# Optimization experiments

Hardware: AMD Instinct MI355X
Metric: run time of the kernel (lower is better)

## Reference

```python
import jax, jax.numpy as jnp
import numpy as np

N_NODES = 100000
N_EDGES = 1600000  # directed, src < dst; to_undirected doubles them
N_GRAPHS = 128
D_IN, D_H, D_FC, N_CLS = 128, 64, 32, 10


def setup_inputs() -> dict:
    key = jax.random.key(0)
    ks = jax.random.split(key, 12)
    x = jax.random.normal(ks[0], (N_NODES, D_IN), dtype=jnp.float32)
    # edges with src < dst so concatenating the flipped copy yields the undirected set
    r = jax.random.randint(ks[1], (2, N_EDGES), 0, N_NODES, dtype=jnp.int64)
    src = jnp.minimum(r[0], r[1])
    dst = jnp.maximum(r[0], r[1])
    dst = jnp.where(src == dst, (dst + 1) % N_NODES, dst)  # avoid pre-existing self loops
    edge_index = jnp.stack([src, dst])
    batch = jnp.sort(jax.random.randint(ks[2], (N_NODES,), 0, N_GRAPHS, dtype=jnp.int64))
    sc = lambda f: 1.0 / jnp.sqrt(jnp.float32(f))
    return {
        "x": x,
        "edge_index": edge_index,
        "batch": batch,
        "W_in": jax.random.normal(ks[3], (D_IN, D_H), jnp.float32) * sc(D_IN),
        "b_in": jnp.zeros((D_H,), jnp.float32),
        "W1": jax.random.normal(ks[4], (D_H, D_H), jnp.float32) * sc(D_H),
        "b1": jnp.zeros((D_H,), jnp.float32),
        "W2": jax.random.normal(ks[5], (D_H, D_H), jnp.float32) * sc(D_H),
        "b2": jnp.zeros((D_H,), jnp.float32),
        "Wf1": jax.random.normal(ks[6], (D_H, D_FC), jnp.float32) * sc(D_H),
        "bf1": jnp.zeros((D_FC,), jnp.float32),
        "Wf2": jax.random.normal(ks[7], (D_FC, N_CLS), jnp.float32) * sc(D_FC),
        "bf2": jnp.zeros((N_CLS,), jnp.float32),
    }


def _gcn_conv(x, W, b, src, dst, dinv, n_nodes):
    # GCNConv: x' = D^{-1/2}(A+I)D^{-1/2} (xW) + b, dinv = deg^{-1/2} incl. self loops
    xw = x @ W
    norm = (dinv[src] * dinv[dst])[:, None]              # [E,1]
    agg = jax.ops.segment_sum(xw[src] * norm, dst, num_segments=n_nodes)
    agg = agg + xw * (dinv * dinv)[:, None]              # self-loop term
    return agg + b


def reference(x, edge_index, batch, W_in, b_in, W1, b1, W2, b2, Wf1, bf1, Wf2, bf2):
    n = x.shape[0]
    # to_undirected: append reversed edges (inputs have src<dst, so no dup dirs)
    src = jnp.concatenate([edge_index[0], edge_index[1]])
    dst = jnp.concatenate([edge_index[1], edge_index[0]])
    # degree including self loop
    deg = 1.0 + jax.ops.segment_sum(jnp.ones_like(dst, dtype=x.dtype), dst, num_segments=n)
    dinv = jax.lax.rsqrt(deg)

    h = jax.nn.relu(x @ W_in + b_in)
    h = jax.nn.relu(_gcn_conv(h, W1, b1, src, dst, dinv, n))
    h = jax.nn.relu(_gcn_conv(h, W2, b2, src, dst, dinv, n))

    # global_mean_pool over graph ids
    sums = jax.ops.segment_sum(h, batch, num_segments=N_GRAPHS)
    cnts = jax.ops.segment_sum(jnp.ones((n,), h.dtype), batch, num_segments=N_GRAPHS)
    pooled = sums / jnp.maximum(cnts, 1.0)[:, None]

    g = jax.nn.relu(pooled @ Wf1 + bf1)
    logits = g @ Wf2 + bf2
    return jax.nn.log_softmax(logits, axis=1)
```

## Files before the change

kernel.cpp:

```cpp
#include <hip/hip_runtime.h>
#include <hip/hip_fp16.h>
#include <math.h>

constexpr int DG  = 128;
constexpr int DIN = 128;
constexpr int DH  = 64;
constexpr int DFC = 32;
constexpr int DC  = 10;
constexpr int CAP  = 80;
constexpr int NPB  = 64;
constexpr int NB   = 1563;
constexpr int ABLK = 256;
constexpr int SCAP = 2560;

typedef _Float16 f16;
typedef f16  f16x8 __attribute__((ext_vector_type(8)));
typedef float f32x4 __attribute__((ext_vector_type(4)));

__device__ __forceinline__ int swz(int row, int byte_in_row) {
    return row * 128 + (byte_in_row ^ ((row & 7) << 4));
}

__global__ __launch_bounds__(256) void k_hist(const int* __restrict__ src,
                                              const int* __restrict__ dst,
                                              int* __restrict__ histT,
                                              int E, int EPB) {
    __shared__ int h[NB];
    for (int i = threadIdx.x; i < NB; i += 256) h[i] = 0;
    __syncthreads();
    int e0 = blockIdx.x * EPB, e1 = min(e0 + EPB, E);
    for (int i = e0 + threadIdx.x; i < e1; i += 256) {
        int u = src[i], v = dst[i];
        atomicAdd(&h[v >> 6], 1);
        atomicAdd(&h[u >> 6], 1);
    }
    __syncthreads();
    for (int i = threadIdx.x; i < NB; i += 256)
        histT[(size_t)i * ABLK + blockIdx.x] = h[i];
}

__global__ __launch_bounds__(256) void k_expand(const int* __restrict__ histT,
                                                int* __restrict__ baseT,
                                                int* __restrict__ ecnt,
                                                float* __restrict__ sums,
                                                int* __restrict__ cnts) {
    __shared__ int s[256];
    int b = blockIdx.x, t = threadIdx.x;
    int v = histT[(size_t)b * ABLK + t];
    s[t] = v;
    __syncthreads();
    for (int o = 1; o < 256; o <<= 1) {
        int tv = (t >= o) ? s[t - o] : 0;
        __syncthreads();
        s[t] += tv;
        __syncthreads();
    }
    int incl = s[t];
    baseT[(size_t)b * ABLK + t] = b * SCAP + incl - v;
    if (t == 255) ecnt[b] = min(incl, SCAP);
    int gid = b * 256 + t;
    if (gid < DG * DH) sums[gid] = 0.0f;
    if (gid < DG) cnts[gid] = 0;
}

__global__ __launch_bounds__(256) void k_binplace(const int* __restrict__ src,
                                                  const int* __restrict__ dst,
                                                  const int* __restrict__ baseT,
                                                  int* __restrict__ staging,
                                                  int E, int EPB) {
    __shared__ int lcnt[NB];
    __shared__ int lbase[NB];
    int blk = blockIdx.x;
    for (int i = threadIdx.x; i < NB; i += 256) {
        lcnt[i]  = 0;
        lbase[i] = baseT[(size_t)i * ABLK + blk];
    }
    __syncthreads();
    int e0 = blk * EPB, e1 = min(e0 + EPB, E);
    for (int i = e0 + threadIdx.x; i < e1; i += 256) {
        int u = src[i], v = dst[i];
        int bv = v >> 6, bu = u >> 6;
        int rv = atomicAdd(&lcnt[bv], 1);
        int sv = lbase[bv] + rv;
        if (sv < (bv + 1) * SCAP) staging[sv] = ((v & 63) << 17) | u;
        int ru = atomicAdd(&lcnt[bu], 1);
        int su = lbase[bu] + ru;
        if (su < (bu + 1) * SCAP) staging[su] = ((u & 63) << 17) | v;
    }
}

__global__ __launch_bounds__(256) void k_rows(const int* __restrict__ staging,
                                              const int* __restrict__ ecnt,
                                              int* __restrict__ adj,
                                              int* __restrict__ cnt,
                                              float* __restrict__ dinv,
                                              int N) {
    __shared__ int rows[NPB * CAP];
    __shared__ int cur[NPB];
    int b = blockIdx.x;
    int nbase = b * NPB;
    int nn = min(NPB, N - nbase);
    if (nn <= 0) return;
    for (int i = threadIdx.x; i < nn; i += 256) cur[i] = 0;
    __syncthreads();
    int s0 = b * SCAP, s1 = s0 + ecnt[b];
    for (int i = s0 + threadIdx.x; i < s1; i += 256) {
        int e  = staging[i];
        int vl = e >> 17;
        int u  = e & 0x1FFFF;
        int p  = atomicAdd(&cur[vl], 1);
        if (p < CAP) rows[vl * CAP + p] = u;
    }
    __syncthreads();
    for (int s = threadIdx.x; s < nn * CAP; s += 256) {
        int node = s / CAP, p = s - node * CAP;
        if (p < min(cur[node], CAP))
            adj[(size_t)(nbase + node) * CAP + p] = rows[s];
    }
    for (int i = threadIdx.x; i < nn; i += 256) {
        int c = cur[i];
        cnt[nbase + i]  = c;
        dinv[nbase + i] = rsqrtf(1.0f + (float)c);
    }
}

__global__ __launch_bounds__(256) void k_wprep(const float* __restrict__ Wi,
                                               const float* __restrict__ W1,
                                               const float* __restrict__ W2,
                                               f16* __restrict__ WiT,
                                               f16* __restrict__ W1T,
                                               f16* __restrict__ W2T) {
    int t = blockIdx.x * 256 + threadIdx.x;
    int stride = gridDim.x * 256;
    for (int i = t; i < DH * DIN; i += stride) {
        int c = i >> 7, k = i & 127;
        WiT[i] = (f16)Wi[k * DH + c];
    }
    for (int i = t; i < DH * DH; i += stride) {
        int c = i >> 6, k = i & 63;
        W1T[i] = (f16)W1[k * DH + c];
        W2T[i] = (f16)W2[k * DH + c];
    }
}

__global__ __launch_bounds__(256) void k_lin2(const float* __restrict__ x,
                                              const f16* __restrict__ WiT,
                                              const float* __restrict__ bi,
                                              const f16* __restrict__ W1T,
                                              const float* __restrict__ dinv,
                                              __half* __restrict__ out, int n) {
    __shared__ f16 h0[4 * 16 * 64];
    int t = threadIdx.x, lane = t & 63, w = t >> 6;
    int rb = blockIdx.x * 64 + w * 16;
    if (rb >= n) return;
    int lr = lane & 15;
    int lg = lane >> 4;
    f16x8 a[4];
    const float* xrow = x + (size_t)(rb + lr) * DIN + lg * 8;
#pragma unroll
    for (int k0 = 0; k0 < 4; k0++) {
        float4 f0 = *(const float4*)(xrow + k0 * 32);
        float4 f1 = *(const float4*)(xrow + k0 * 32 + 4);
        a[k0][0] = (f16)f0.x; a[k0][1] = (f16)f0.y; a[k0][2] = (f16)f0.z; a[k0][3] = (f16)f0.w;
        a[k0][4] = (f16)f1.x; a[k0][5] = (f16)f1.y; a[k0][6] = (f16)f1.z; a[k0][7] = (f16)f1.w;
    }
    char* hwb = (char*)(h0 + w * 16 * 64);
#pragma unroll
    for (int cb = 0; cb < 4; cb++) {
        f32x4 acc = {0.f, 0.f, 0.f, 0.f};
        const f16* wt = WiT + (cb * 16 + lr) * DIN + lg * 8;
#pragma unroll
        for (int k0 = 0; k0 < 4; k0++) {
            f16x8 bf = *(const f16x8*)(wt + k0 * 32);
            acc = __builtin_amdgcn_mfma_f32_16x16x32_f16(a[k0], bf, acc, 0, 0, 0);
        }
        float bv = bi[cb * 16 + lr];
#pragma unroll
        for (int r = 0; r < 4; r++) {
            int row = lg * 4 + r;
            *(f16*)(hwb + swz(row, (cb * 16 + lr) * 2)) = (f16)fmaxf(acc[r] + bv, 0.0f);
        }
    }
    f16x8 a2[2];
#pragma unroll
    for (int k0 = 0; k0 < 2; k0++)
        a2[k0] = *(const f16x8*)(hwb + swz(lr, k0 * 64 + lg * 16));
    float dv[4];
#pragma unroll
    for (int r = 0; r < 4; r++) dv[r] = dinv[rb + lg * 4 + r];
#pragma unroll
    for (int cb = 0; cb < 4; cb++) {
        f32x4 acc = {0.f, 0.f, 0.f, 0.f};
        const f16* wt = W1T + (cb * 16 + lr) * DH + lg * 8;
        acc = __builtin_amdgcn_mfma_f32_16x16x32_f16(a2[0], *(const f16x8*)(wt), acc, 0, 0, 0);
        acc = __builtin_amdgcn_mfma_f32_16x16x32_f16(a2[1], *(const f16x8*)(wt + 32), acc, 0, 0, 0);
#pragma unroll
        for (int r = 0; r < 4; r++)
            out[(size_t)(rb + lg * 4 + r) * DH + cb * 16 + lr] = __float2half(acc[r] * dv[r]);
    }
}

__device__ __forceinline__ void gather_node(int v, const int* __restrict__ cnt,
                                            const int* __restrict__ adj,
                                            const char* __restrict__ xb,
                                            int lane, int half_id, int fpo,
                                            float& ax, float& ay) {
    int len = min(cnt[v], CAP);
    const int* row = adj + (size_t)v * CAP;
    int idx = 0;
    if (lane < len) idx = row[lane];
    int len64 = min(len, 64);
    ax = 0.f; ay = 0.f;
    int k = half_id;
    for (; k + 14 < len64; k += 16) {
        int u0 = __shfl(idx, k);
        int u1 = __shfl(idx, k + 2);
        int u2 = __shfl(idx, k + 4);
        int u3 = __shfl(idx, k + 6);
        int u4 = __shfl(idx, k + 8);
        int u5 = __shfl(idx, k + 10);
        int u6 = __shfl(idx, k + 12);
        int u7 = __shfl(idx, k + 14);
        __half2 h0 = *(const __half2*)(xb + ((u0 << 7) | fpo));
        __half2 h1 = *(const __half2*)(xb + ((u1 << 7) | fpo));
        __half2 h2 = *(const __half2*)(xb + ((u2 << 7) | fpo));
        __half2 h3 = *(const __half2*)(xb + ((u3 << 7) | fpo));
        h0 = __hadd2(h0, *(const __half2*)(xb + ((u4 << 7) | fpo)));
        h1 = __hadd2(h1, *(const __half2*)(xb + ((u5 << 7) | fpo)));
        h2 = __hadd2(h2, *(const __half2*)(xb + ((u6 << 7) | fpo)));
        h3 = __hadd2(h3, *(const __half2*)(xb + ((u7 << 7) | fpo)));
        float2 f0 = __half22float2(h0);
        float2 f1 = __half22float2(h1);
        float2 f2 = __half22float2(h2);
        float2 f3 = __half22float2(h3);
        ax += (f0.x + f1.x) + (f2.x + f3.x);
        ay += (f0.y + f1.y) + (f2.y + f3.y);
    }
    for (; k < len64; k += 2) {
        int u0 = __shfl(idx, k);
        float2 f0 = __half22float2(*(const __half2*)(xb + ((u0 << 7) | fpo)));
        ax += f0.x; ay += f0.y;
    }
    for (int j = 64 + half_id; j < len; j += 2) {
        float2 f0 = __half22float2(*(const __half2*)(xb + ((row[j] << 7) | fpo)));
        ax += f0.x; ay += f0.y;
    }
    ax += __shfl_xor(ax, 32);
    ay += __shfl_xor(ay, 32);
}

__global__ __launch_bounds__(64) void k_g1(const int* __restrict__ cnt,
                                           const int* __restrict__ adj,
                                           const __half2* __restrict__ xws,
                                           const float* __restrict__ dinv,
                                           const float* __restrict__ b,
                                           const f16* __restrict__ W2T,
                                           __half* __restrict__ out, int n) {
    __shared__ char wb[2048];
    int lane = threadIdx.x & 63;
    int rb = blockIdx.x * 16;
    if (rb >= n) return;
    int half_id = lane >> 5, fp = lane & 31, fpo = fp << 2;
    const char* xb = (const char*)xws;
    float2 bb = ((const float2*)b)[fp];
#pragma unroll 1
    for (int i = 0; i < 16; i++) {
        int v = rb + i;
        float ax, ay;
        gather_node(v, cnt, adj, xb, lane, half_id, fpo, ax, ay);
        if (half_id == 0) {
            float2 s  = __half22float2(*(const __half2*)(xb + ((v << 7) | fpo)));
            float  dv = dinv[v];
            __half2 hh = __floats2half2_rn(fmaxf(dv * (ax + s.x) + bb.x, 0.0f),
                                           fmaxf(dv * (ay + s.y) + bb.y, 0.0f));
            *(__half2*)(wb + swz(i, fpo)) = hh;
        }
    }
    int lr = lane & 15, lg = lane >> 4;
    f16x8 a0 = *(const f16x8*)(wb + swz(lr, lg * 16));
    f16x8 a1 = *(const f16x8*)(wb + swz(lr, 64 + lg * 16));
    float dvr[4];
#pragma unroll
    for (int r = 0; r < 4; r++) dvr[r] = dinv[rb + lg * 4 + r];
#pragma unroll
    for (int cb = 0; cb < 4; cb++) {
        const f16* wt = W2T + (cb * 16 + lr) * DH + lg * 8;
        f32x4 acc = {0.f, 0.f, 0.f, 0.f};
        acc = __builtin_amdgcn_mfma_f32_16x16x32_f16(a0, *(const f16x8*)(wt), acc, 0, 0, 0);
        acc = __builtin_amdgcn_mfma_f32_16x16x32_f16(a1, *(const f16x8*)(wt + 32), acc, 0, 0, 0);
#pragma unroll
        for (int r = 0; r < 4; r++)
            out[(size_t)(rb + lg * 4 + r) * DH + cb * 16 + lr] = __float2half(acc[r] * dvr[r]);
    }
}

__global__ __launch_bounds__(64) void k_g2(const int* __restrict__ cnt,
                                           const int* __restrict__ adj,
                                           const __half2* __restrict__ xws,
                                           const float* __restrict__ dinv,
                                           const float* __restrict__ b,
                                           const int* __restrict__ batch,
                                           float* __restrict__ sums,
                                           int* __restrict__ cnts, int n) {
    int lane = threadIdx.x & 63;
    int rb = blockIdx.x * 16;
    if (rb >= n) return;
    int half_id = lane >> 5, fp = lane & 31, fpo = fp << 2;
    const char* xb = (const char*)xws;
    float2 bb = ((const float2*)b)[fp];
    int curg = -1, c = 0;
    float pax = 0.f, pay = 0.f;
#pragma unroll 1
    for (int i = 0; i < 16; i++) {
        int v = rb + i;
        float ax, ay;
        gather_node(v, cnt, adj, xb, lane, half_id, fpo, ax, ay);
        float2 s  = __half22float2(*(const __half2*)(xb + ((v << 7) | fpo)));
        float  dv = dinv[v];
        float ox = fmaxf(dv * (ax + s.x) + bb.x, 0.0f);
        float oy = fmaxf(dv * (ay + s.y) + bb.y, 0.0f);
        int g = batch[v];
        if (g != curg) {
            if (curg >= 0 && half_id == 0) {
                atomicAdd(&sums[curg * DH + 2 * fp],     pax);
                atomicAdd(&sums[curg * DH + 2 * fp + 1], pay);
                if (lane == 0) atomicAdd(&cnts[curg], c);
            }
            curg = g; pax = 0.f; pay = 0.f; c = 0;
        }
        if (half_id == 0) { pax += ox; pay += oy; }
        c++;
    }
    if (curg >= 0 && half_id == 0) {
        atomicAdd(&sums[curg * DH + 2 * fp],     pax);
        atomicAdd(&sums[curg * DH + 2 * fp + 1], pay);
        if (lane == 0) atomicAdd(&cnts[curg], c);
    }
}

__global__ __launch_bounds__(64) void k_head(const float* __restrict__ sums,
                                             const int* __restrict__ cnts,
                                             const float* __restrict__ Wf1,
                                             const float* __restrict__ bf1,
                                             const float* __restrict__ Wf2,
                                             const float* __restrict__ bf2,
                                             float* __restrict__ out) {
    int g = blockIdx.x, lane = threadIdx.x;
    float cnt    = (float)max(cnts[g], 1);
    float pooled = sums[g * DH + lane] / cnt;
    float acc = (lane < DFC) ? bf1[lane] : 0.f;
    for (int k = 0; k < DH; k++) {
        float pk = __shfl(pooled, k);
        if (lane < DFC) acc = fmaf(pk, Wf1[k * DFC + lane], acc);
    }
    float gv = fmaxf(acc, 0.f);
    float acc2 = (lane < DC) ? bf2[lane] : 0.f;
    for (int k = 0; k < DFC; k++) {
        float gk = __shfl(gv, k);
        if (lane < DC) acc2 = fmaf(gk, Wf2[k * DC + lane], acc2);
    }
    float v = (lane < DC) ? acc2 : -INFINITY;
    float m = v;
    for (int o = 8; o; o >>= 1) m = fmaxf(m, __shfl_xor(m, o));
    float e = (lane < DC) ? expf(v - m) : 0.f;
    float s = e;
    for (int o = 8; o; o >>= 1) s += __shfl_xor(s, o);
    if (lane < DC) out[g * DC + lane] = v - m - logf(s);
}

extern "C" void kernel_launch(void* const* d_in, const int* in_sizes, int n_in,
                              void* d_out, int out_size, void* d_ws, size_t ws_size,
                              hipStream_t stream) {
    const float* x    = (const float*)d_in[0];
    const int*   ei   = (const int*)d_in[1];
    const int*   batch= (const int*)d_in[2];
    const float* W_in = (const float*)d_in[3];
    const float* b_in = (const float*)d_in[4];
    const float* W1   = (const float*)d_in[5];
    const float* b1   = (const float*)d_in[6];
    const float* W2   = (const float*)d_in[7];
    const float* b2   = (const float*)d_in[8];
    const float* Wf1  = (const float*)d_in[9];
    const float* bf1  = (const float*)d_in[10];
    const float* Wf2  = (const float*)d_in[11];
    const float* bf2  = (const float*)d_in[12];
    float* out = (float*)d_out;

    const int E = in_sizes[1] / 2;
    const int N = in_sizes[0] / DIN;
    const int* src = ei;
    const int* dst = ei + E;

    const int NBU = (N + NPB - 1) / NPB;
    const int EPB = (E + ABLK - 1) / ABLK;

    char* ws = (char*)d_ws;
    size_t off = 0;
    auto alloc = [&](size_t bytes) -> void* {
        void* p = ws + off;
        off = (off + bytes + 255) & ~(size_t)255;
        return p;
    };
    int*    cnt     = (int*)   alloc((size_t)N * 4);
    float*  dinv    = (float*) alloc((size_t)N * 4);
    int*    adj     = (int*)   alloc((size_t)N * CAP * 4);
    int*    histT   = (int*)   alloc((size_t)NB * ABLK * 4);
    int*    baseT   = (int*)   alloc((size_t)NB * ABLK * 4);
    int*    ecnt    = (int*)   alloc((size_t)NB * 4);
    int*    staging = (int*)   alloc((size_t)NB * SCAP * 4);
    __half* hA      = (__half*)alloc((size_t)N * DH * 2);
    __half* hX      = (__half*)alloc((size_t)N * DH * 2);
    float*  sums    = (float*) alloc((size_t)DG * DH * 4);
    int*    cnts    = (int*)   alloc((size_t)DG * 4);
    f16*    WiT     = (f16*)   alloc((size_t)DH * DIN * 2);
    f16*    W1T     = (f16*)   alloc((size_t)DH * DH * 2);
    f16*    W2T     = (f16*)   alloc((size_t)DH * DH * 2);

    k_wprep<<<32, 256, 0, stream>>>(W_in, W1, W2, WiT, W1T, W2T);

    k_hist<<<ABLK, 256, 0, stream>>>(src, dst, histT, E, EPB);
    k_expand<<<NB, 256, 0, stream>>>(histT, baseT, ecnt, sums, cnts);
    k_binplace<<<ABLK, 256, 0, stream>>>(src, dst, baseT, staging, E, EPB);
    k_rows<<<NBU, 256, 0, stream>>>(staging, ecnt, adj, cnt, dinv, N);

    k_lin2<<<(N + 63) / 64, 256, 0, stream>>>(x, WiT, b_in, W1T, dinv, hX, N);

    k_g1<<<(N + 15) / 16, 64, 0, stream>>>(cnt, adj, (const __half2*)hX, dinv, b1, W2T, hA, N);

    k_g2<<<(N + 15) / 16, 64, 0, stream>>>(cnt, adj, (const __half2*)hA, dinv, b2, batch, sums, cnts, N);

    k_head<<<DG, 64, 0, stream>>>(sums, cnts, Wf1, bf1, Wf2, bf2, out);
}
```

Before: 262.6 us.

## Fold weight prep into expand kernel and spread g1 rows across four waves

```diff
diff --git a/kernel.cpp b/kernel.cpp
--- a/kernel.cpp
+++ b/kernel.cpp
@@ -43,7 +43,13 @@
                                                 int* __restrict__ baseT,
                                                 int* __restrict__ ecnt,
                                                 float* __restrict__ sums,
-                                                int* __restrict__ cnts) {
+                                                int* __restrict__ cnts,
+                                                const float* __restrict__ Wi,
+                                                const float* __restrict__ W1,
+                                                const float* __restrict__ W2,
+                                                f16* __restrict__ WiT,
+                                                f16* __restrict__ W1T,
+                                                f16* __restrict__ W2T) {
     __shared__ int s[256];
     int b = blockIdx.x, t = threadIdx.x;
     int v = histT[(size_t)b * ABLK + t];
@@ -61,6 +67,15 @@
     int gid = b * 256 + t;
     if (gid < DG * DH) sums[gid] = 0.0f;
     if (gid < DG) cnts[gid] = 0;
+    if (gid < DH * DIN) {
+        int c = gid >> 7, k = gid & 127;
+        WiT[gid] = (f16)Wi[k * DH + c];
+    }
+    if (gid < DH * DH) {
+        int c = gid >> 6, k = gid & 63;
+        W1T[gid] = (f16)W1[k * DH + c];
+        W2T[gid] = (f16)W2[k * DH + c];
+    }
 }
 
 __global__ __launch_bounds__(256) void k_binplace(const int* __restrict__ src,
@@ -121,25 +136,6 @@
         int c = cur[i];
         cnt[nbase + i]  = c;
         dinv[nbase + i] = rsqrtf(1.0f + (float)c);
-    }
-}
-
-__global__ __launch_bounds__(256) void k_wprep(const float* __restrict__ Wi,
-                                               const float* __restrict__ W1,
-                                               const float* __restrict__ W2,
-                                               f16* __restrict__ WiT,
-                                               f16* __restrict__ W1T,
-                                               f16* __restrict__ W2T) {
-    int t = blockIdx.x * 256 + threadIdx.x;
-    int stride = gridDim.x * 256;
-    for (int i = t; i < DH * DIN; i += stride) {
-        int c = i >> 7, k = i & 127;
-        WiT[i] = (f16)Wi[k * DH + c];
-    }
-    for (int i = t; i < DH * DH; i += stride) {
-        int c = i >> 6, k = i & 63;
-        W1T[i] = (f16)W1[k * DH + c];
-        W2T[i] = (f16)W2[k * DH + c];
     }
 }
 
@@ -249,23 +245,24 @@
     ay += __shfl_xor(ay, 32);
 }
 
-__global__ __launch_bounds__(64) void k_g1(const int* __restrict__ cnt,
-                                           const int* __restrict__ adj,
-                                           const __half2* __restrict__ xws,
-                                           const float* __restrict__ dinv,
-                                           const float* __restrict__ b,
-                                           const f16* __restrict__ W2T,
-                                           __half* __restrict__ out, int n) {
+__global__ __launch_bounds__(256) void k_g1(const int* __restrict__ cnt,
+                                            const int* __restrict__ adj,
+                                            const __half2* __restrict__ xws,
+                                            const float* __restrict__ dinv,
+                                            const float* __restrict__ b,
+                                            const f16* __restrict__ W2T,
+                                            __half* __restrict__ out, int n) {
     __shared__ char wb[2048];
-    int lane = threadIdx.x & 63;
+    int t = threadIdx.x, lane = t & 63, w = t >> 6;
     int rb = blockIdx.x * 16;
     if (rb >= n) return;
     int half_id = lane >> 5, fp = lane & 31, fpo = fp << 2;
     const char* xb = (const char*)xws;
     float2 bb = ((const float2*)b)[fp];
 #pragma unroll 1
-    for (int i = 0; i < 16; i++) {
-        int v = rb + i;
+    for (int i = 0; i < 4; i++) {
+        int row = w * 4 + i;
+        int v = rb + row;
         float ax, ay;
         gather_node(v, cnt, adj, xb, lane, half_id, fpo, ax, ay);
         if (half_id == 0) {
@@ -273,25 +270,24 @@
             float  dv = dinv[v];
             __half2 hh = __floats2half2_rn(fmaxf(dv * (ax + s.x) + bb.x, 0.0f),
                                            fmaxf(dv * (ay + s.y) + bb.y, 0.0f));
-            *(__half2*)(wb + swz(i, fpo)) = hh;
+            *(__half2*)(wb + swz(row, fpo)) = hh;
         }
     }
+    __syncthreads();
     int lr = lane & 15, lg = lane >> 4;
     f16x8 a0 = *(const f16x8*)(wb + swz(lr, lg * 16));
     f16x8 a1 = *(const f16x8*)(wb + swz(lr, 64 + lg * 16));
     float dvr[4];
 #pragma unroll
     for (int r = 0; r < 4; r++) dvr[r] = dinv[rb + lg * 4 + r];
-#pragma unroll
-    for (int cb = 0; cb < 4; cb++) {
-        const f16* wt = W2T + (cb * 16 + lr) * DH + lg * 8;
-        f32x4 acc = {0.f, 0.f, 0.f, 0.f};
-        acc = __builtin_amdgcn_mfma_f32_16x16x32_f16(a0, *(const f16x8*)(wt), acc, 0, 0, 0);
-        acc = __builtin_amdgcn_mfma_f32_16x16x32_f16(a1, *(const f16x8*)(wt + 32), acc, 0, 0, 0);
-#pragma unroll
-        for (int r = 0; r < 4; r++)
-            out[(size_t)(rb + lg * 4 + r) * DH + cb * 16 + lr] = __float2half(acc[r] * dvr[r]);
-    }
+    int cb = w;
+    const f16* wt = W2T + (cb * 16 + lr) * DH + lg * 8;
+    f32x4 acc = {0.f, 0.f, 0.f, 0.f};
+    acc = __builtin_amdgcn_mfma_f32_16x16x32_f16(a0, *(const f16x8*)(wt), acc, 0, 0, 0);
+    acc = __builtin_amdgcn_mfma_f32_16x16x32_f16(a1, *(const f16x8*)(wt + 32), acc, 0, 0, 0);
+#pragma unroll
+    for (int r = 0; r < 4; r++)
+        out[(size_t)(rb + lg * 4 + r) * DH + cb * 16 + lr] = __float2half(acc[r] * dvr[r]);
 }
 
 __global__ __launch_bounds__(64) void k_g2(const int* __restrict__ cnt,
@@ -416,16 +412,15 @@
     f16*    W1T     = (f16*)   alloc((size_t)DH * DH * 2);
     f16*    W2T     = (f16*)   alloc((size_t)DH * DH * 2);
 
-    k_wprep<<<32, 256, 0, stream>>>(W_in, W1, W2, WiT, W1T, W2T);
-
     k_hist<<<ABLK, 256, 0, stream>>>(src, dst, histT, E, EPB);
-    k_expand<<<NB, 256, 0, stream>>>(histT, baseT, ecnt, sums, cnts);
+    k_expand<<<NB, 256, 0, stream>>>(histT, baseT, ecnt, sums, cnts,
+                                     W_in, W1, W2, WiT, W1T, W2T);
     k_binplace<<<ABLK, 256, 0, stream>>>(src, dst, baseT, staging, E, EPB);
     k_rows<<<NBU, 256, 0, stream>>>(staging, ecnt, adj, cnt, dinv, N);
 
     k_lin2<<<(N + 63) / 64, 256, 0, stream>>>(x, WiT, b_in, W1T, dinv, hX, N);
 
-    k_g1<<<(N + 15) / 16, 64, 0, stream>>>(cnt, adj, (const __half2*)hX, dinv, b1, W2T, hA, N);
+    k_g1<<<(N + 15) / 16, 256, 0, stream>>>(cnt, adj, (const __half2*)hX, dinv, b1, W2T, hA, N);
 
     k_g2<<<(N + 15) / 16, 64, 0, stream>>>(cnt, adj, (const __half2*)hA, dinv, b2, batch, sums, cnts, N);
 
```

New measurement: 256.8 us. -2.2%, faster.
